# Kernel tuning notes

Hardware: AMD Instinct MI355X
Metric: run time of the kernel (lower is better)

Reference implementation:

```python
import jax, jax.numpy as jnp
import numpy as np

B, S, H, R = 4, 1024, 1024, 32


def setup_inputs() -> dict:
    key = jax.random.key(0)
    k1, k2, k3 = jax.random.split(key, 3)
    hidden_states = jax.random.normal(k1, (B, S, H), dtype=jnp.float32)
    # full cartesian grid of (seq_idx, hidden_idx), as required by the final
    # out.view(B, S, H, 1) reshape in the original module
    n = jnp.arange(S * H, dtype=jnp.int64)
    all_indices = jnp.stack([n // H, n % H], axis=1)  # [S*H, 2]
    # Linear weights, torch layout [out_features, in_features], scaled like kaiming-uniform-ish
    seq_W = jax.random.normal(k2, (R, H), dtype=jnp.float32) / np.sqrt(H)
    hid_W = jax.random.normal(k3, (R, S), dtype=jnp.float32) / np.sqrt(S)
    cp_weight = jnp.ones((1, R), dtype=jnp.float32)  # frozen all-ones CP mixing weight
    return {"hidden_states": hidden_states, "all_indices": all_indices,
            "seq_W": seq_W, "hid_W": hid_W, "cp_weight": cp_weight}


def reference(hidden_states, all_indices, seq_W, hid_W, cp_weight):
    # seq-mode factor: Linear(H -> R) over [B, S, H] -> [B, S, R]
    seq_emb = jnp.einsum('bsh,rh->bsr', hidden_states, seq_W)
    # hidden-mode factor: Linear(S -> R) over transposed [B, H, S] -> [B, H, R]
    hid_emb = jnp.einsum('bsh,rs->bhr', hidden_states, hid_W)
    s_idx = all_indices[:, 0]  # [N]
    h_idx = all_indices[:, 1]  # [N]
    g_seq = seq_emb[:, s_idx, :]  # [B, N, R] gather along seq axis
    g_hid = hid_emb[:, h_idx, :]  # [B, N, R] gather along hidden axis
    # hadamard + rank reduction with (frozen) CP weight; out_units == 1 squeezed
    out = jnp.einsum('bnr,bnr,r->bn', g_seq, g_hid, cp_weight[0])
    return out.reshape(B, S, H)
```

## Files before the change

### kernel.cpp

```cpp
#include <hip/hip_runtime.h>

typedef __attribute__((ext_vector_type(8))) short bf16x8;
typedef __attribute__((ext_vector_type(4))) float f32x4;
typedef __attribute__((ext_vector_type(2))) float f32x2;
typedef __attribute__((ext_vector_type(4))) short short4v;

__device__ __forceinline__ unsigned short f2bf(float x) {
    union { __bf16 h; unsigned short s; } u;
    u.h = (__bf16)x;
    return u.s;
}

__global__ __launch_bounds__(256) void gemm_fused(
    const float* __restrict__ hs, const float* __restrict__ seqW,
    const float* __restrict__ hidW, const float* __restrict__ cpw,
    unsigned short* __restrict__ E16 )
{
    __shared__ short wpk[32768];
    __shared__ float red[4][16][32];

    const int bid = blockIdx.x;
    const bool hid = bid >= 256;
    const int mt  = hid ? bid - 256 : bid;
    const int tid = threadIdx.x;
    const int wv  = tid >> 6;
    const int l   = tid & 63;
    const int l15 = l & 15;
    const int g   = l >> 4;
    const int m0  = mt * 16;
    const int mrow = m0 + l15;

    const float* __restrict__ W = hid ? hidW : seqW;
    size_t arow;
    if (hid) arow = ((size_t)(mrow >> 10) << 20) + (size_t)(mrow & 1023);
    else     arow = (size_t)mrow << 10;
    const int kbase = wv * 256;

    {
        const int kstep = tid >> 3;
        const int gg    = (tid >> 1) & 3;
        const int half  = tid & 1;
        #pragma unroll 4
        for (int row = 0; row < 32; ++row) {
            f32x4 v = *(const f32x4*)(W + (size_t)row * 1024 + tid * 4);
            short4v h4 = { (short)f2bf(v.x), (short)f2bf(v.y),
                           (short)f2bf(v.z), (short)f2bf(v.w) };
            const int frag = (row >> 4) * 2048 + kstep * 64 + gg * 16 + (row & 15);
            *(short4v*)&wpk[frag * 8 + half * 4] = h4;
        }
    }

    float a[64];
    if (hid) {
        const float* pa = hs + arow + (size_t)(kbase + g * 8) * 1024;
        #pragma unroll
        for (int ks = 0; ks < 8; ++ks)
            #pragma unroll
            for (int j = 0; j < 8; ++j)
                a[ks * 8 + j] = pa[(size_t)(ks * 32 + j) * 1024];
    } else {
        const f32x4* pa = (const f32x4*)(hs + arow + kbase + g * 8);
        #pragma unroll
        for (int ks = 0; ks < 8; ++ks) {
            f32x4 v0 = pa[ks * 8];
            f32x4 v1 = pa[ks * 8 + 1];
            a[ks*8+0]=v0.x; a[ks*8+1]=v0.y; a[ks*8+2]=v0.z; a[ks*8+3]=v0.w;
            a[ks*8+4]=v1.x; a[ks*8+5]=v1.y; a[ks*8+6]=v1.z; a[ks*8+7]=v1.w;
        }
    }

    __syncthreads();

    f32x4 acc0 = {0.f,0.f,0.f,0.f}, acc1 = {0.f,0.f,0.f,0.f};
    #pragma unroll
    for (int ks = 0; ks < 8; ++ks) {
        const int kstep = wv * 8 + ks;
        bf16x8 af, bf0, bf1;
        #pragma unroll
        for (int j = 0; j < 8; ++j) af[j] = (short)f2bf(a[ks * 8 + j]);
        bf0 = *(const bf16x8*)&wpk[(kstep * 64 + g * 16 + l15) * 8];
        bf1 = *(const bf16x8*)&wpk[(2048 + kstep * 64 + g * 16 + l15) * 8];
        acc0 = __builtin_amdgcn_mfma_f32_16x16x32_bf16(af, bf0, acc0, 0, 0, 0);
        acc1 = __builtin_amdgcn_mfma_f32_16x16x32_bf16(af, bf1, acc1, 0, 0, 0);
    }

    #pragma unroll
    for (int r = 0; r < 4; ++r) {
        red[wv][4 * g + r][l15]      = acc0[r];
        red[wv][4 * g + r][l15 + 16] = acc1[r];
    }
    __syncthreads();

    const int o = tid * 2;
    const float* rf = &red[0][0][0];
    float vx = rf[o]     + rf[512 + o]     + rf[1024 + o]     + rf[1536 + o];
    float vy = rf[o + 1] + rf[512 + o + 1] + rf[1024 + o + 1] + rf[1536 + o + 1];
    if (!hid) {
        f32x2 w = *(const f32x2*)(cpw + (o & 31));
        vx *= w.x; vy *= w.y;
    }
    unsigned pk = (unsigned)f2bf(vx) | ((unsigned)f2bf(vy) << 16);
    unsigned short* Eo = E16 + (hid ? (size_t)4096 * 32 : 0) + (size_t)m0 * 32 + o;
    *(unsigned*)Eo = pk;
}

__global__ __launch_bounds__(256) void k3(const unsigned short* __restrict__ E16,
                                          float* __restrict__ out)
{
    const int tid = threadIdx.x;
    const int wv  = tid >> 6;
    const int l   = tid & 63;
    const int l15 = l & 15;
    const int g   = l >> 4;
    const int b   = blockIdx.z;
    const int s0  = blockIdx.y * 64 + wv * 16;
    const int h0  = blockIdx.x * 64;

    const unsigned short* As = E16 + ((size_t)(b * 1024 + s0)) * 32;
    const unsigned short* Bh = E16 + (size_t)4096 * 32 + ((size_t)(b * 1024 + h0)) * 32;

    bf16x8 af = *(const bf16x8*)(As + (size_t)l15 * 32 + g * 8);
    bf16x8 bfr[4];
    #pragma unroll
    for (int j = 0; j < 4; ++j)
        bfr[j] = *(const bf16x8*)(Bh + (size_t)(4 * l15 + j) * 32 + g * 8);

    const f32x4 zero = {0.f, 0.f, 0.f, 0.f};
    f32x4 acc[4];
    #pragma unroll
    for (int j = 0; j < 4; ++j)
        acc[j] = __builtin_amdgcn_mfma_f32_16x16x32_bf16(af, bfr[j], zero, 0, 0, 0);

    #pragma unroll
    for (int r = 0; r < 4; ++r) {
        f32x4 v = { acc[0][r], acc[1][r], acc[2][r], acc[3][r] };
        float* orow = out + ((size_t)(b * 1024 + s0 + 4 * g + r)) * 1024 + h0 + 4 * l15;
        __builtin_nontemporal_store(v, (f32x4*)orow);
    }
}

extern "C" void kernel_launch(void* const* d_in, const int* in_sizes, int n_in,
                              void* d_out, int out_size, void* d_ws, size_t ws_size,
                              hipStream_t stream) {
    const float* hs   = (const float*)d_in[0];
    const float* seqW = (const float*)d_in[2];
    const float* hidW = (const float*)d_in[3];
    const float* cpw  = (const float*)d_in[4];
    float* out = (float*)d_out;

    unsigned short* E16 = (unsigned short*)d_ws;

    gemm_fused<<<512, 256, 0, stream>>>(hs, seqW, hidW, cpw, E16);
    dim3 grid3(16, 16, 4);
    k3<<<grid3, 256, 0, stream>>>(E16, out);
}
```

Baseline: 20.77 us.

## Split GEMM K dimension across two blocks and sum partials in k3

The projection GEMM now splits the 1024-long reduction into two K-chunks, launching twice as many blocks (1024). Each block holds half the weights in shared memory and half the A registers, which is meant to raise occupancy and parallelism across the CUs. The two bf16 partial results are written to separate workspace halves and added in k3 before the MFMA. The cost is an extra bf16 rounding step, doubled partial reads in k3, and more weight-conversion work overall.

```diff
diff --git a/kernel.cpp b/kernel.cpp
--- a/kernel.cpp
+++ b/kernel.cpp
@@ -11,17 +11,25 @@
     return u.s;
 }
 
+__device__ __forceinline__ float bf2f(short s) {
+    union { unsigned u; float f; } v;
+    v.u = ((unsigned)(unsigned short)s) << 16;
+    return v.f;
+}
+
 __global__ __launch_bounds__(256) void gemm_fused(
     const float* __restrict__ hs, const float* __restrict__ seqW,
     const float* __restrict__ hidW, const float* __restrict__ cpw,
     unsigned short* __restrict__ E16 )
 {
-    __shared__ short wpk[32768];
+    __shared__ short wpk[16384];
     __shared__ float red[4][16][32];
 
-    const int bid = blockIdx.x;
-    const bool hid = bid >= 256;
-    const int mt  = hid ? bid - 256 : bid;
+    const int bid    = blockIdx.x;
+    const int kchunk = bid >> 9;
+    const int rest   = bid & 511;
+    const bool hid   = rest >= 256;
+    const int mt     = rest & 255;
     const int tid = threadIdx.x;
     const int wv  = tid >> 6;
     const int l   = tid & 63;
@@ -34,34 +42,37 @@
     size_t arow;
     if (hid) arow = ((size_t)(mrow >> 10) << 20) + (size_t)(mrow & 1023);
     else     arow = (size_t)mrow << 10;
-    const int kbase = wv * 256;
+    const int kbase = kchunk * 512 + wv * 128;
 
     {
-        const int kstep = tid >> 3;
-        const int gg    = (tid >> 1) & 3;
-        const int half  = tid & 1;
+        const int rowg = tid >> 7;
+        const int cth  = tid & 127;
+        const int kstep = cth >> 3;
+        const int gg    = (cth >> 1) & 3;
+        const int half  = cth & 1;
         #pragma unroll 4
-        for (int row = 0; row < 32; ++row) {
-            f32x4 v = *(const f32x4*)(W + (size_t)row * 1024 + tid * 4);
+        for (int pass = 0; pass < 16; ++pass) {
+            const int row = pass * 2 + rowg;
+            f32x4 v = *(const f32x4*)(W + (size_t)row * 1024 + kchunk * 512 + cth * 4);
             short4v h4 = { (short)f2bf(v.x), (short)f2bf(v.y),
                            (short)f2bf(v.z), (short)f2bf(v.w) };
-            const int frag = (row >> 4) * 2048 + kstep * 64 + gg * 16 + (row & 15);
+            const int frag = (row >> 4) * 1024 + kstep * 64 + gg * 16 + (row & 15);
             *(short4v*)&wpk[frag * 8 + half * 4] = h4;
         }
     }
 
-    float a[64];
+    float a[32];
     if (hid) {
         const float* pa = hs + arow + (size_t)(kbase + g * 8) * 1024;
         #pragma unroll
-        for (int ks = 0; ks < 8; ++ks)
+        for (int ks = 0; ks < 4; ++ks)
             #pragma unroll
             for (int j = 0; j < 8; ++j)
                 a[ks * 8 + j] = pa[(size_t)(ks * 32 + j) * 1024];
     } else {
         const f32x4* pa = (const f32x4*)(hs + arow + kbase + g * 8);
         #pragma unroll
-        for (int ks = 0; ks < 8; ++ks) {
+        for (int ks = 0; ks < 4; ++ks) {
             f32x4 v0 = pa[ks * 8];
             f32x4 v1 = pa[ks * 8 + 1];
             a[ks*8+0]=v0.x; a[ks*8+1]=v0.y; a[ks*8+2]=v0.z; a[ks*8+3]=v0.w;
@@ -73,13 +84,13 @@
 
     f32x4 acc0 = {0.f,0.f,0.f,0.f}, acc1 = {0.f,0.f,0.f,0.f};
     #pragma unroll
-    for (int ks = 0; ks < 8; ++ks) {
-        const int kstep = wv * 8 + ks;
-        bf16x8 af, bf0, bf1;
+    for (int ks = 0; ks < 4; ++ks) {
+        const int kstep = wv * 4 + ks;
+        bf16x8 af;
         #pragma unroll
         for (int j = 0; j < 8; ++j) af[j] = (short)f2bf(a[ks * 8 + j]);
-        bf0 = *(const bf16x8*)&wpk[(kstep * 64 + g * 16 + l15) * 8];
-        bf1 = *(const bf16x8*)&wpk[(2048 + kstep * 64 + g * 16 + l15) * 8];
+        bf16x8 bf0 = *(const bf16x8*)&wpk[(kstep * 64 + g * 16 + l15) * 8];
+        bf16x8 bf1 = *(const bf16x8*)&wpk[(1024 + kstep * 64 + g * 16 + l15) * 8];
         acc0 = __builtin_amdgcn_mfma_f32_16x16x32_bf16(af, bf0, acc0, 0, 0, 0);
         acc1 = __builtin_amdgcn_mfma_f32_16x16x32_bf16(af, bf1, acc1, 0, 0, 0);
     }
@@ -100,8 +111,18 @@
         vx *= w.x; vy *= w.y;
     }
     unsigned pk = (unsigned)f2bf(vx) | ((unsigned)f2bf(vy) << 16);
-    unsigned short* Eo = E16 + (hid ? (size_t)4096 * 32 : 0) + (size_t)m0 * 32 + o;
+    unsigned short* Eo = E16 + (size_t)kchunk * (2 * 4096 * 32)
+                             + (hid ? (size_t)4096 * 32 : 0)
+                             + (size_t)m0 * 32 + o;
     *(unsigned*)Eo = pk;
+}
+
+__device__ __forceinline__ bf16x8 sum2(bf16x8 x, bf16x8 y) {
+    bf16x8 r;
+    #pragma unroll
+    for (int j = 0; j < 8; ++j)
+        r[j] = (short)f2bf(bf2f(x[j]) + bf2f(y[j]));
+    return r;
 }
 
 __global__ __launch_bounds__(256) void k3(const unsigned short* __restrict__ E16,
@@ -116,14 +137,17 @@
     const int s0  = blockIdx.y * 64 + wv * 16;
     const int h0  = blockIdx.x * 64;
 
-    const unsigned short* As = E16 + ((size_t)(b * 1024 + s0)) * 32;
-    const unsigned short* Bh = E16 + (size_t)4096 * 32 + ((size_t)(b * 1024 + h0)) * 32;
+    const size_t CH = (size_t)2 * 4096 * 32;
+    const unsigned short* As0 = E16 + ((size_t)(b * 1024 + s0)) * 32;
+    const unsigned short* Bh0 = E16 + (size_t)4096 * 32 + ((size_t)(b * 1024 + h0)) * 32;
 
-    bf16x8 af = *(const bf16x8*)(As + (size_t)l15 * 32 + g * 8);
+    bf16x8 af = sum2(*(const bf16x8*)(As0 + (size_t)l15 * 32 + g * 8),
+                     *(const bf16x8*)(As0 + CH + (size_t)l15 * 32 + g * 8));
     bf16x8 bfr[4];
     #pragma unroll
     for (int j = 0; j < 4; ++j)
-        bfr[j] = *(const bf16x8*)(Bh + (size_t)(4 * l15 + j) * 32 + g * 8);
+        bfr[j] = sum2(*(const bf16x8*)(Bh0 + (size_t)(4 * l15 + j) * 32 + g * 8),
+                      *(const bf16x8*)(Bh0 + CH + (size_t)(4 * l15 + j) * 32 + g * 8));
 
     const f32x4 zero = {0.f, 0.f, 0.f, 0.f};
     f32x4 acc[4];
@@ -150,7 +174,7 @@
 
     unsigned short* E16 = (unsigned short*)d_ws;
 
-    gemm_fused<<<512, 256, 0, stream>>>(hs, seqW, hidW, cpw, E16);
+    gemm_fused<<<1024, 256, 0, stream>>>(hs, seqW, hidW, cpw, E16);
     dim3 grid3(16, 16, 4);
     k3<<<grid3, 256, 0, stream>>>(E16, out);
 }
```

Result: slower. 24.69 us (+18.9%).
